# Kernel tuning notes

Measured on AMD Instinct MI355X. Metric: run time of the kernel, lower is better.

Reference implementation:

```python
import jax, jax.numpy as jnp
import numpy as np

TOPK = 8
EPS = 1e-12  # F.normalize eps


def setup_inputs() -> dict:
    key = jax.random.key(0)
    k1, k2 = jax.random.split(key)
    feats = jax.random.normal(k1, (4, 256, 64, 64), dtype=jnp.float32)
    logits = jax.random.normal(k2, (4, 1, 64, 64), dtype=jnp.float32)
    return {"feats": feats, "logits": logits}


def reference(feats, logits):
    b, c, h, w = feats.shape
    n = h * w
    feat_flat = feats.reshape(b, c, n)
    # F.normalize(dim=1): x / max(||x||_2, eps)
    norm = jnp.sqrt(jnp.sum(feat_flat * feat_flat, axis=1, keepdims=True))
    feat_norm = feat_flat / jnp.maximum(norm, EPS)
    # sim[b,i,j] = <f_i, f_j>  -> [B, N, N]
    sim = jnp.einsum('bci,bcj->bij', feat_norm, feat_norm)
    k = min(TOPK, n)
    _, idx = jax.lax.top_k(sim, k)  # [B, N, k] indices
    prob = jax.nn.sigmoid(logits).reshape(b, n)  # [B, N]
    # gathered[b,i,j] = prob[b, idx[b,i,j]]
    gathered = jax.vmap(lambda p, i: p[i])(prob, idx)  # [B, N, k]
    anchor = prob[:, :, None]  # [B, N, 1] broadcast over k
    loss = jnp.mean(jnp.abs(anchor - gathered))
    return loss
```

## Files before the change

### kernel.cpp

```cpp
#include <hip/hip_runtime.h>
#include <hip/hip_bf16.h>

typedef _Float16 half8 __attribute__((ext_vector_type(8)));
typedef unsigned short ushort8 __attribute__((ext_vector_type(8)));
typedef float floatx4 __attribute__((ext_vector_type(4)));

#define B_ 4
#define C_ 256
#define N_ 4096
#define NT 32
#define TRI 528

#define OFF_FN    ((size_t)0)
#define OFF_PROB  ((size_t)(8u << 20))
#define OFF_PART  (OFF_PROB + 65536)
#define OFF_TOP   ((size_t)(16u << 20))

__device__ __forceinline__ void gl_lds16(const void* g, void* l) {
    __builtin_amdgcn_global_load_lds(
        (const __attribute__((address_space(1))) void*)g,
        (__attribute__((address_space(3))) void*)l,
        16, 0, 0);
}

__device__ __forceinline__ void cas(uint32_t& a, uint32_t& b) {
    uint32_t hi = max(a, b); b = min(a, b); a = hi;
}

__device__ __forceinline__ void sort8(uint32_t v[8]) {
    cas(v[0],v[1]); cas(v[2],v[3]); cas(v[4],v[5]); cas(v[6],v[7]);
    cas(v[0],v[2]); cas(v[1],v[3]); cas(v[4],v[6]); cas(v[5],v[7]);
    cas(v[1],v[2]); cas(v[5],v[6]);
    cas(v[0],v[4]); cas(v[1],v[5]); cas(v[2],v[6]); cas(v[3],v[7]);
    cas(v[2],v[4]); cas(v[3],v[5]);
    cas(v[1],v[2]); cas(v[3],v[4]); cas(v[5],v[6]);
}

__device__ __forceinline__ void merge8(uint32_t r[8], const uint32_t n[8]) {
    uint32_t m[8];
#pragma unroll
    for (int i = 0; i < 8; ++i) m[i] = max(r[i], n[7 - i]);
    cas(m[0],m[4]); cas(m[1],m[5]); cas(m[2],m[6]); cas(m[3],m[7]);
    cas(m[0],m[2]); cas(m[1],m[3]); cas(m[4],m[6]); cas(m[5],m[7]);
    cas(m[0],m[1]); cas(m[2],m[3]); cas(m[4],m[5]); cas(m[6],m[7]);
#pragma unroll
    for (int i = 0; i < 8; ++i) r[i] = m[i];
}

#define TS 68
__global__ __launch_bounds__(256) void prep_kernel(const float* __restrict__ feats,
                                                   const float* __restrict__ logits,
                                                   _Float16* __restrict__ fn,
                                                   float* __restrict__ prob) {
    __shared__ __align__(16) float T[C_ * TS];
    __shared__ float S[256];
    __shared__ float I[64];

    const int t  = threadIdx.x;
    const int b  = blockIdx.x >> 6;
    const int i0 = (blockIdx.x & 63) * 64;
    const float* fb = feats + (size_t)b * C_ * N_;

#pragma unroll
    for (int k = 0; k < 16; ++k) {
        int ch = t + k * 256;
        int row = ch >> 4, col4 = ch & 15;
        float4 v = *(const float4*)(fb + (size_t)row * N_ + i0 + col4 * 4);
        *(float4*)&T[row * TS + col4 * 4] = v;
    }
    __syncthreads();
    {
        int i = t & 63, cq = t >> 6;
        float ss = 0.f;
#pragma unroll 8
        for (int j = 0; j < 64; ++j) { float v = T[(cq * 64 + j) * TS + i]; ss += v * v; }
        S[cq * 64 + i] = ss;
    }
    __syncthreads();
    if (t < 64) {
        float ss = S[t] + S[64 + t] + S[128 + t] + S[192 + t];
        I[t] = 1.f / fmaxf(sqrtf(ss), 1e-12f);
        float lg = logits[b * N_ + i0 + t];
        prob[b * N_ + i0 + t] = 1.f / (1.f + expf(-lg));
    }
    __syncthreads();
    {
        int i = t >> 2, chunk = t & 3;
        float s = I[i];
        _Float16* fr = fn + ((size_t)(b * N_ + i0 + i)) * C_ + chunk * 64;
#pragma unroll
        for (int v8 = 0; v8 < 8; ++v8) {
            half8 h;
#pragma unroll
            for (int e = 0; e < 8; ++e)
                h[e] = (_Float16)(T[(chunk * 64 + v8 * 8 + e) * TS + i] * s);
            *(half8*)(fr + v8 * 8) = h;
        }
    }
}

#define CSH 136
__global__ __launch_bounds__(256, 3) void gram_sel_kernel(const _Float16* __restrict__ fn,
                                                          uint32_t* __restrict__ top) {
    __shared__ __align__(16) char smem[128 * CSH * 2];
    _Float16* As = (_Float16*)smem;
    _Float16* Bs = (_Float16*)(smem + 16384);
    unsigned short* Ch = (unsigned short*)smem;
    uint32_t* Ms = (uint32_t*)smem;

    const int t    = threadIdx.x;
    const int lane = t & 63;
    const int w    = t >> 6;
    const int m16  = lane & 15;
    const int q    = lane >> 4;

    const int b = blockIdx.x / TRI;
    const int u = blockIdx.x - b * TRI;
    int it = (int)(32.5f - sqrtf(32.5f * 32.5f - 2.0f * (float)u));
    while (u >= (it + 1) * (65 - (it + 1)) / 2) ++it;
    while (u < it * (65 - it) / 2) --it;
    const int jt = it + (u - it * (65 - it) / 2);
    const bool diag = (it == jt);

    const int i0 = it * 128, j0 = jt * 128;
    const _Float16* fnb = fn + (size_t)b * N_ * C_;

    const int srowb = t >> 3;
    const int schunk = (t & 7) ^ (srowb & 7);
    const int sw = m16 & 7;

    floatx4 acc[2][8];
#pragma unroll
    for (int ri = 0; ri < 2; ++ri)
#pragma unroll
        for (int jj = 0; jj < 8; ++jj) acc[ri][jj] = floatx4{0.f, 0.f, 0.f, 0.f};

    for (int kc = 0; kc < 4; ++kc) {
#pragma unroll
        for (int r = 0; r < 4; ++r) {
            int row = r * 32 + srowb;
            const _Float16* gA = fnb + (size_t)(i0 + row) * C_ + kc * 64 + schunk * 8;
            const _Float16* gB = fnb + (size_t)(j0 + row) * C_ + kc * 64 + schunk * 8;
            gl_lds16(gA, (char*)As + r * 4096 + t * 16);
            gl_lds16(gB, (char*)Bs + r * 4096 + t * 16);
        }
        __syncthreads();
#pragma unroll
        for (int kk = 0; kk < 2; ++kk) {
            half8 a0 = *(const half8*)&As[(w * 32 + m16) * 64 + ((kk * 4 + q) ^ sw) * 8];
            half8 a1 = *(const half8*)&As[(w * 32 + 16 + m16) * 64 + ((kk * 4 + q) ^ sw) * 8];
#pragma unroll
            for (int jj = 0; jj < 8; ++jj) {
                half8 bf = *(const half8*)&Bs[(jj * 16 + m16) * 64 + ((kk * 4 + q) ^ sw) * 8];
                acc[0][jj] = __builtin_amdgcn_mfma_f32_16x16x32_f16(a0, bf, acc[0][jj], 0, 0, 0);
                acc[1][jj] = __builtin_amdgcn_mfma_f32_16x16x32_f16(a1, bf, acc[1][jj], 0, 0, 0);
            }
        }
        __syncthreads();
    }

#pragma unroll
    for (int jj = 0; jj < 8; ++jj)
#pragma unroll
        for (int ri = 0; ri < 2; ++ri) {
            const int col = jj * 16 + m16;
            const int row = w * 32 + ri * 16 + q * 4;
#pragma unroll
            for (int p = 0; p < 2; ++p) {
                auto pk2 = __builtin_amdgcn_cvt_pkrtz(acc[ri][jj][2 * p], acc[ri][jj][2 * p + 1]);
                uint32_t bits = __builtin_bit_cast(uint32_t, pk2);
                uint32_t s = (bits >> 15) & 0x00010001u;
                uint32_t fl = bits ^ (s * 0x7FFFu + 0x80008000u);
                *(uint32_t*)&Ch[col * CSH + row + 2 * p] = fl;
            }
        }
    __syncthreads();

    uint32_t cpk[8], rpk[8];
    {
        const int ccol = t >> 1, cr0 = (t & 1) * 64;
        const unsigned short* cc = &Ch[ccol * CSH + cr0];
        const int ibase = i0 + cr0;
#pragma unroll
        for (int g = 0; g < 8; ++g) {
            ushort8 v = *(const ushort8*)(cc + g * 8);
            uint32_t cand[8];
#pragma unroll
            for (int e = 0; e < 8; ++e)
                cand[e] = ((uint32_t)v[e] << 16) | (uint32_t)(ibase + g * 8 + e);
            sort8(cand);
            if (g == 0) {
#pragma unroll
                for (int s = 0; s < 8; ++s) cpk[s] = cand[s];
            } else merge8(cpk, cand);
        }
    }
    if (!diag) {
        const int rrow = t >> 1, ch0 = (t & 1) * 64;
        const unsigned short* cr = &Ch[ch0 * CSH + rrow];
        const int jbase = j0 + ch0;
#pragma unroll
        for (int g = 0; g < 8; ++g) {
            uint32_t cand[8];
#pragma unroll
            for (int e = 0; e < 8; ++e)
                cand[e] = ((uint32_t)cr[(g * 8 + e) * CSH] << 16) | (uint32_t)(jbase + g * 8 + e);
            sort8(cand);
            if (g == 0) {
#pragma unroll
                for (int s = 0; s < 8; ++s) rpk[s] = cand[s];
            } else merge8(rpk, cand);
        }
    }
    __syncthreads();

    if (t & 1) {
#pragma unroll
        for (int s = 0; s < 8; ++s) Ms[(t >> 1) * 8 + s] = cpk[s];
        if (!diag) {
#pragma unroll
            for (int s = 0; s < 8; ++s) Ms[1024 + (t >> 1) * 8 + s] = rpk[s];
        }
    }
    __syncthreads();
    if (!(t & 1)) {
        uint32_t o[8];
#pragma unroll
        for (int s = 0; s < 8; ++s) o[s] = Ms[(t >> 1) * 8 + s];
        merge8(cpk, o);
        uint32_t* dst = top + (((size_t)b * N_ + j0 + (t >> 1)) * 32 + it) * 8;
        *(uint4*)dst       = make_uint4(cpk[0], cpk[1], cpk[2], cpk[3]);
        *(uint4*)(dst + 4) = make_uint4(cpk[4], cpk[5], cpk[6], cpk[7]);
        if (!diag) {
#pragma unroll
            for (int s = 0; s < 8; ++s) o[s] = Ms[1024 + (t >> 1) * 8 + s];
            merge8(rpk, o);
            uint32_t* dst2 = top + (((size_t)b * N_ + i0 + (t >> 1)) * 32 + jt) * 8;
            *(uint4*)dst2       = make_uint4(rpk[0], rpk[1], rpk[2], rpk[3]);
            *(uint4*)(dst2 + 4) = make_uint4(rpk[4], rpk[5], rpk[6], rpk[7]);
        }
    }
}

__global__ __launch_bounds__(256) void merge_kernel(const uint32_t* __restrict__ top,
                                                    const float* __restrict__ prob,
                                                    float* __restrict__ partials) {
    __shared__ float red[4];
    const int t = threadIdx.x;
    const int lane = t & 63;
    const int w = t >> 6;
    const int rg = blockIdx.x * 4 + w;
    const int b = rg >> 12;

    uint4 v4 = ((const uint4*)(top + (size_t)rg * 256))[lane];
    uint32_t v[4] = {v4.x, v4.y, v4.z, v4.w};
    uint32_t m = max(max(v[0], v[1]), max(v[2], v[3]));

    const float* pb = prob + (b << 12);
    float p_r = prob[rg];
    float contrib = 0.f;
#pragma unroll
    for (int k = 0; k < 8; ++k) {
        uint32_t M = m;
#pragma unroll
        for (int off = 32; off; off >>= 1) M = max(M, (uint32_t)__shfl_xor((int)M, off));
        if (lane == k) contrib = fabsf(p_r - pb[M & 0xFFFu]);
#pragma unroll
        for (int s = 0; s < 4; ++s) v[s] = (v[s] == M) ? 0u : v[s];
        m = max(max(v[0], v[1]), max(v[2], v[3]));
    }
#pragma unroll
    for (int off = 32; off; off >>= 1) contrib += __shfl_xor(contrib, off);
    if (lane == 0) red[w] = contrib;
    __syncthreads();
    if (t == 0) partials[blockIdx.x] = red[0] + red[1] + red[2] + red[3];
}

__global__ __launch_bounds__(256) void final_kernel(const float* __restrict__ partials,
                                                    float* __restrict__ out) {
    __shared__ float red[256];
    int t = threadIdx.x;
    float s = 0.f;
#pragma unroll
    for (int k = 0; k < 16; ++k) s += partials[k * 256 + t];
    red[t] = s;
    __syncthreads();
    for (int off = 128; off > 0; off >>= 1) {
        if (t < off) red[t] += red[t + off];
        __syncthreads();
    }
    if (t == 0) out[0] = red[0] * (1.f / (B_ * N_ * 8.0f));
}

extern "C" void kernel_launch(void* const* d_in, const int* in_sizes, int n_in,
                              void* d_out, int out_size, void* d_ws, size_t ws_size,
                              hipStream_t stream) {
    const float* feats  = (const float*)d_in[0];
    const float* logits = (const float*)d_in[1];
    float* out = (float*)d_out;
    char* ws = (char*)d_ws;
    _Float16* fn   = (_Float16*)(ws + OFF_FN);
    float* prob    = (float*)(ws + OFF_PROB);
    float* parts   = (float*)(ws + OFF_PART);
    uint32_t* top  = (uint32_t*)(ws + OFF_TOP);

    prep_kernel<<<256, 256, 0, stream>>>(feats, logits, fn, prob);
    gram_sel_kernel<<<B_ * TRI, 256, 0, stream>>>(fn, top);
    merge_kernel<<<4096, 256, 0, stream>>>(top, prob, parts);
    final_kernel<<<1, 256, 0, stream>>>(parts, out);
}
```

Measured before the change: 125.1 us.

## Balance gram tile work by packing off-diagonal and diagonal tiles per block

Replaces one-tile-per-block scheduling (2112 blocks) with 1024 persistent-style blocks. Blocks 0-959 each process two off-diagonal tiles, and blocks 960-1023 process two diagonal tiles plus one off-diagonal tile, so each block does roughly equal selection work. The column and row top-k passes for off-diagonal tiles are interleaved in one loop to expose more instruction-level parallelism. The cost is that each block now runs its tiles sequentially with no overlap of loads, and extra register pressure from the interleaved sorts could hurt occupancy.

```diff
diff --git a/kernel.cpp b/kernel.cpp
--- a/kernel.cpp
+++ b/kernel.cpp
@@ -9,7 +9,8 @@
 #define C_ 256
 #define N_ 4096
 #define NT 32
-#define TRI 528
+#define NOD 496
+#define NDG 32
 
 #define OFF_FN    ((size_t)0)
 #define OFF_PROB  ((size_t)(8u << 20))
@@ -114,130 +115,153 @@
     const int m16  = lane & 15;
     const int q    = lane >> 4;
 
-    const int b = blockIdx.x / TRI;
-    const int u = blockIdx.x - b * TRI;
-    int it = (int)(32.5f - sqrtf(32.5f * 32.5f - 2.0f * (float)u));
-    while (u >= (it + 1) * (65 - (it + 1)) / 2) ++it;
-    while (u < it * (65 - it) / 2) --it;
-    const int jt = it + (u - it * (65 - it) / 2);
-    const bool diag = (it == jt);
-
-    const int i0 = it * 128, j0 = jt * 128;
-    const _Float16* fnb = fn + (size_t)b * N_ * C_;
+    const int g = blockIdx.x;
+    const int ntile = (g < 960) ? 2 : 3;
 
     const int srowb = t >> 3;
     const int schunk = (t & 7) ^ (srowb & 7);
     const int sw = m16 & 7;
 
-    floatx4 acc[2][8];
-#pragma unroll
-    for (int ri = 0; ri < 2; ++ri)
-#pragma unroll
-        for (int jj = 0; jj < 8; ++jj) acc[ri][jj] = floatx4{0.f, 0.f, 0.f, 0.f};
-
-    for (int kc = 0; kc < 4; ++kc) {
-#pragma unroll
-        for (int r = 0; r < 4; ++r) {
-            int row = r * 32 + srowb;
-            const _Float16* gA = fnb + (size_t)(i0 + row) * C_ + kc * 64 + schunk * 8;
-            const _Float16* gB = fnb + (size_t)(j0 + row) * C_ + kc * 64 + schunk * 8;
-            gl_lds16(gA, (char*)As + r * 4096 + t * 16);
-            gl_lds16(gB, (char*)Bs + r * 4096 + t * 16);
-        }
-        __syncthreads();
-#pragma unroll
-        for (int kk = 0; kk < 2; ++kk) {
-            half8 a0 = *(const half8*)&As[(w * 32 + m16) * 64 + ((kk * 4 + q) ^ sw) * 8];
-            half8 a1 = *(const half8*)&As[(w * 32 + 16 + m16) * 64 + ((kk * 4 + q) ^ sw) * 8];
-#pragma unroll
-            for (int jj = 0; jj < 8; ++jj) {
-                half8 bf = *(const half8*)&Bs[(jj * 16 + m16) * 64 + ((kk * 4 + q) ^ sw) * 8];
-                acc[0][jj] = __builtin_amdgcn_mfma_f32_16x16x32_f16(a0, bf, acc[0][jj], 0, 0, 0);
-                acc[1][jj] = __builtin_amdgcn_mfma_f32_16x16x32_f16(a1, bf, acc[1][jj], 0, 0, 0);
-            }
-        }
-        __syncthreads();
-    }
-
-#pragma unroll
-    for (int jj = 0; jj < 8; ++jj)
-#pragma unroll
-        for (int ri = 0; ri < 2; ++ri) {
-            const int col = jj * 16 + m16;
-            const int row = w * 32 + ri * 16 + q * 4;
-#pragma unroll
-            for (int p = 0; p < 2; ++p) {
-                auto pk2 = __builtin_amdgcn_cvt_pkrtz(acc[ri][jj][2 * p], acc[ri][jj][2 * p + 1]);
-                uint32_t bits = __builtin_bit_cast(uint32_t, pk2);
-                uint32_t s = (bits >> 15) & 0x00010001u;
-                uint32_t fl = bits ^ (s * 0x7FFFu + 0x80008000u);
-                *(uint32_t*)&Ch[col * CSH + row + 2 * p] = fl;
-            }
-        }
-    __syncthreads();
-
-    uint32_t cpk[8], rpk[8];
-    {
-        const int ccol = t >> 1, cr0 = (t & 1) * 64;
-        const unsigned short* cc = &Ch[ccol * CSH + cr0];
-        const int ibase = i0 + cr0;
-#pragma unroll
-        for (int g = 0; g < 8; ++g) {
-            ushort8 v = *(const ushort8*)(cc + g * 8);
-            uint32_t cand[8];
-#pragma unroll
-            for (int e = 0; e < 8; ++e)
-                cand[e] = ((uint32_t)v[e] << 16) | (uint32_t)(ibase + g * 8 + e);
-            sort8(cand);
-            if (g == 0) {
-#pragma unroll
-                for (int s = 0; s < 8; ++s) cpk[s] = cand[s];
-            } else merge8(cpk, cand);
-        }
-    }
-    if (!diag) {
-        const int rrow = t >> 1, ch0 = (t & 1) * 64;
-        const unsigned short* cr = &Ch[ch0 * CSH + rrow];
-        const int jbase = j0 + ch0;
-#pragma unroll
-        for (int g = 0; g < 8; ++g) {
-            uint32_t cand[8];
-#pragma unroll
-            for (int e = 0; e < 8; ++e)
-                cand[e] = ((uint32_t)cr[(g * 8 + e) * CSH] << 16) | (uint32_t)(jbase + g * 8 + e);
-            sort8(cand);
-            if (g == 0) {
-#pragma unroll
-                for (int s = 0; s < 8; ++s) rpk[s] = cand[s];
-            } else merge8(rpk, cand);
-        }
-    }
-    __syncthreads();
-
-    if (t & 1) {
-#pragma unroll
-        for (int s = 0; s < 8; ++s) Ms[(t >> 1) * 8 + s] = cpk[s];
-        if (!diag) {
-#pragma unroll
-            for (int s = 0; s < 8; ++s) Ms[1024 + (t >> 1) * 8 + s] = rpk[s];
-        }
-    }
-    __syncthreads();
-    if (!(t & 1)) {
-        uint32_t o[8];
-#pragma unroll
-        for (int s = 0; s < 8; ++s) o[s] = Ms[(t >> 1) * 8 + s];
-        merge8(cpk, o);
-        uint32_t* dst = top + (((size_t)b * N_ + j0 + (t >> 1)) * 32 + it) * 8;
-        *(uint4*)dst       = make_uint4(cpk[0], cpk[1], cpk[2], cpk[3]);
-        *(uint4*)(dst + 4) = make_uint4(cpk[4], cpk[5], cpk[6], cpk[7]);
-        if (!diag) {
-#pragma unroll
-            for (int s = 0; s < 8; ++s) o[s] = Ms[1024 + (t >> 1) * 8 + s];
-            merge8(rpk, o);
-            uint32_t* dst2 = top + (((size_t)b * N_ + i0 + (t >> 1)) * 32 + jt) * 8;
-            *(uint4*)dst2       = make_uint4(rpk[0], rpk[1], rpk[2], rpk[3]);
-            *(uint4*)(dst2 + 4) = make_uint4(rpk[4], rpk[5], rpk[6], rpk[7]);
+    for (int ti = 0; ti < ntile; ++ti) {
+        int b, it, jt; bool diag;
+        int u = -1;
+        if (g < 960) u = 2 * g + ti;
+        else if (ti == 2) u = 1920 + (g - 960);
+        if (u >= 0) {
+            b = u / NOD;
+            int od = u - b * NOD;
+            int itg = (int)(31.5f - sqrtf(31.5f * 31.5f - 2.0f * (float)od));
+            if (itg < 0) itg = 0; if (itg > 30) itg = 30;
+            while (itg < 30 && od >= (itg + 1) * (63 - (itg + 1)) / 2) ++itg;
+            while (itg > 0 && od < itg * (63 - itg) / 2) --itg;
+            it = itg;
+            jt = it + 1 + (od - it * (63 - it) / 2);
+            diag = false;
+        } else {
+            int d = 2 * (g - 960) + ti;
+            b = d >> 5; it = jt = d & 31;
+            diag = true;
+        }
+        const int i0 = it * 128, j0 = jt * 128;
+        const _Float16* fnb = fn + (size_t)b * N_ * C_;
+
+        __syncthreads();
+
+        floatx4 acc[2][8];
+#pragma unroll
+        for (int ri = 0; ri < 2; ++ri)
+#pragma unroll
+            for (int jj = 0; jj < 8; ++jj) acc[ri][jj] = floatx4{0.f, 0.f, 0.f, 0.f};
+
+        for (int kc = 0; kc < 4; ++kc) {
+#pragma unroll
+            for (int r = 0; r < 4; ++r) {
+                int row = r * 32 + srowb;
+                const _Float16* gA = fnb + (size_t)(i0 + row) * C_ + kc * 64 + schunk * 8;
+                const _Float16* gB = fnb + (size_t)(j0 + row) * C_ + kc * 64 + schunk * 8;
+                gl_lds16(gA, (char*)As + r * 4096 + t * 16);
+                gl_lds16(gB, (char*)Bs + r * 4096 + t * 16);
+            }
+            __syncthreads();
+#pragma unroll
+            for (int kk = 0; kk < 2; ++kk) {
+                half8 a0 = *(const half8*)&As[(w * 32 + m16) * 64 + ((kk * 4 + q) ^ sw) * 8];
+                half8 a1 = *(const half8*)&As[(w * 32 + 16 + m16) * 64 + ((kk * 4 + q) ^ sw) * 8];
+#pragma unroll
+                for (int jj = 0; jj < 8; ++jj) {
+                    half8 bf = *(const half8*)&Bs[(jj * 16 + m16) * 64 + ((kk * 4 + q) ^ sw) * 8];
+                    acc[0][jj] = __builtin_amdgcn_mfma_f32_16x16x32_f16(a0, bf, acc[0][jj], 0, 0, 0);
+                    acc[1][jj] = __builtin_amdgcn_mfma_f32_16x16x32_f16(a1, bf, acc[1][jj], 0, 0, 0);
+                }
+            }
+            __syncthreads();
+        }
+
+#pragma unroll
+        for (int jj = 0; jj < 8; ++jj)
+#pragma unroll
+            for (int ri = 0; ri < 2; ++ri) {
+                const int col = jj * 16 + m16;
+                const int row = w * 32 + ri * 16 + q * 4;
+#pragma unroll
+                for (int p = 0; p < 2; ++p) {
+                    auto pk2 = __builtin_amdgcn_cvt_pkrtz(acc[ri][jj][2 * p], acc[ri][jj][2 * p + 1]);
+                    uint32_t bits = __builtin_bit_cast(uint32_t, pk2);
+                    uint32_t s = (bits >> 15) & 0x00010001u;
+                    uint32_t fl = bits ^ (s * 0x7FFFu + 0x80008000u);
+                    *(uint32_t*)&Ch[col * CSH + row + 2 * p] = fl;
+                }
+            }
+        __syncthreads();
+
+        uint32_t cpk[8], rpk[8];
+        {
+            const int ccol = t >> 1, cr0 = (t & 1) * 64;
+            const unsigned short* cc = &Ch[ccol * CSH + cr0];
+            const int ibase = i0 + cr0;
+            const int rrow = t >> 1, ch0 = (t & 1) * 64;
+            const unsigned short* cr = &Ch[ch0 * CSH + rrow];
+            const int jbase = j0 + ch0;
+            if (diag) {
+#pragma unroll
+                for (int g8 = 0; g8 < 8; ++g8) {
+                    ushort8 v = *(const ushort8*)(cc + g8 * 8);
+                    uint32_t cand[8];
+#pragma unroll
+                    for (int e = 0; e < 8; ++e)
+                        cand[e] = ((uint32_t)v[e] << 16) | (uint32_t)(ibase + g8 * 8 + e);
+                    sort8(cand);
+                    if (g8 == 0) {
+#pragma unroll
+                        for (int s = 0; s < 8; ++s) cpk[s] = cand[s];
+                    } else merge8(cpk, cand);
+                }
+            } else {
+#pragma unroll
+                for (int g8 = 0; g8 < 8; ++g8) {
+                    ushort8 v = *(const ushort8*)(cc + g8 * 8);
+                    uint32_t cand[8], cand2[8];
+#pragma unroll
+                    for (int e = 0; e < 8; ++e) {
+                        cand[e]  = ((uint32_t)v[e] << 16) | (uint32_t)(ibase + g8 * 8 + e);
+                        cand2[e] = ((uint32_t)cr[(g8 * 8 + e) * CSH] << 16) | (uint32_t)(jbase + g8 * 8 + e);
+                    }
+                    sort8(cand);
+                    sort8(cand2);
+                    if (g8 == 0) {
+#pragma unroll
+                        for (int s = 0; s < 8; ++s) { cpk[s] = cand[s]; rpk[s] = cand2[s]; }
+                    } else { merge8(cpk, cand); merge8(rpk, cand2); }
+                }
+            }
+        }
+        __syncthreads();
+
+        if (t & 1) {
+#pragma unroll
+            for (int s = 0; s < 8; ++s) Ms[(t >> 1) * 8 + s] = cpk[s];
+            if (!diag) {
+#pragma unroll
+                for (int s = 0; s < 8; ++s) Ms[1024 + (t >> 1) * 8 + s] = rpk[s];
+            }
+        }
+        __syncthreads();
+        if (!(t & 1)) {
+            uint32_t o[8];
+#pragma unroll
+            for (int s = 0; s < 8; ++s) o[s] = Ms[(t >> 1) * 8 + s];
+            merge8(cpk, o);
+            uint32_t* dst = top + (((size_t)b * N_ + j0 + (t >> 1)) * 32 + it) * 8;
+            *(uint4*)dst       = make_uint4(cpk[0], cpk[1], cpk[2], cpk[3]);
+            *(uint4*)(dst + 4) = make_uint4(cpk[4], cpk[5], cpk[6], cpk[7]);
+            if (!diag) {
+#pragma unroll
+                for (int s = 0; s < 8; ++s) o[s] = Ms[1024 + (t >> 1) * 8 + s];
+                merge8(rpk, o);
+                uint32_t* dst2 = top + (((size_t)b * N_ + i0 + (t >> 1)) * 32 + jt) * 8;
+                *(uint4*)dst2       = make_uint4(rpk[0], rpk[1], rpk[2], rpk[3]);
+                *(uint4*)(dst2 + 4) = make_uint4(rpk[4], rpk[5], rpk[6], rpk[7]);
+            }
         }
     }
 }
@@ -305,7 +329,7 @@
     uint32_t* top  = (uint32_t*)(ws + OFF_TOP);
 
     prep_kernel<<<256, 256, 0, stream>>>(feats, logits, fn, prob);
-    gram_sel_kernel<<<B_ * TRI, 256, 0, stream>>>(fn, top);
+    gram_sel_kernel<<<1024, 256, 0, stream>>>(fn, top);
     merge_kernel<<<4096, 256, 0, stream>>>(top, prob, parts);
     final_kernel<<<1, 256, 0, stream>>>(parts, out);
 }
```

After: 130.6 us. 4.4% more time.
